# Kernel optimization log

Hardware: AMD Instinct MI355X
Metric: run time of the kernel (lower is better)

## Reference

```python
import jax, jax.numpy as jnp
import numpy as np

B, S, DIM = 4, 1024, 2048
NH, NKV, HD = 16, 4, 128
G = NH // NKV  # query heads per kv head


def _rope(t, cos, sin):
    # t: (B, S, H, HD); cos/sin: (S, HD//2). Llama-style pairwise rotation.
    tr = t.reshape(*t.shape[:-1], HD // 2, 2)
    t_r, t_i = tr[..., 0], tr[..., 1]
    c = cos[None, :, None, :]
    s = sin[None, :, None, :]
    out_r = t_r * c - t_i * s
    out_i = t_r * s + t_i * c
    return jnp.stack([out_r, out_i], axis=-1).reshape(t.shape)


def setup_inputs() -> dict:
    key = jax.random.key(0)
    ks = jax.random.split(key, 5)
    x = jax.random.normal(ks[0], (B, S, DIM), dtype=jnp.float32)
    # Standard RoPE frequencies
    inv_freq = 1.0 / (10000.0 ** (jnp.arange(0, HD, 2, dtype=jnp.float32) / HD))
    ang = jnp.outer(jnp.arange(S, dtype=jnp.float32), inv_freq)  # (S, HD//2)
    freqs_cos = jnp.cos(ang)
    freqs_sin = jnp.sin(ang)
    # Additive causal mask (1,1,S,S)
    causal = jnp.tril(jnp.ones((S, S), dtype=bool))
    attention_mask = jnp.where(causal, 0.0, -1e9).astype(jnp.float32)[None, None]
    sc = 0.02
    wq = jax.random.normal(ks[1], (NH * HD, DIM), dtype=jnp.float32) * sc
    wk = jax.random.normal(ks[2], (NKV * HD, DIM), dtype=jnp.float32) * sc
    wv = jax.random.normal(ks[3], (NKV * HD, DIM), dtype=jnp.float32) * sc
    wo = jax.random.normal(ks[4], (DIM, NH * HD), dtype=jnp.float32) * sc
    return {"x": x, "freqs_cos": freqs_cos, "freqs_sin": freqs_sin,
            "attention_mask": attention_mask, "wq": wq, "wk": wk, "wv": wv, "wo": wo}


def reference(x, freqs_cos, freqs_sin, attention_mask, wq, wk, wv, wo):
    b, s, _ = x.shape
    q = (x @ wq.T).reshape(b, s, NH, HD)
    k = (x @ wk.T).reshape(b, s, NKV, HD)
    v = (x @ wv.T).reshape(b, s, NKV, HD)
    q = _rope(q, freqs_cos, freqs_sin)
    k = _rope(k, freqs_cos, freqs_sin)
    # kv cache (pre-repeat, as in the torch module)
    new_kv_cache = (k, v)
    # GQA attention: broadcast KV heads across query-head groups instead of
    # materializing repeat_kv (identical math).
    qh = q.transpose(0, 2, 1, 3).reshape(b, NKV, G, s, HD)  # (b, kv, g, s, d)
    kh = k.transpose(0, 2, 1, 3)                             # (b, kv, s, d)
    vh = v.transpose(0, 2, 1, 3)
    scale = 1.0 / jnp.sqrt(jnp.asarray(HD, dtype=x.dtype))
    scores = jnp.einsum('bkgqd,bksd->bkgqs', qh, kh) * scale
    scores = scores + attention_mask[:, :, None]  # (1,1,1,S,S) broadcast
    attn = jax.nn.softmax(scores, axis=-1)
    out = jnp.einsum('bkgqs,bksd->bkgqd', attn, vh)
    out = out.reshape(b, NH, s, HD).transpose(0, 2, 1, 3).reshape(b, s, NH * HD)
    out = out @ wo.T
    return (out, new_kv_cache)
```

## Files before the change

### kernel.cpp

```cpp
#include <hip/hip_runtime.h>

typedef __bf16 bf16;
typedef __bf16 bf16x8 __attribute__((ext_vector_type(8)));
typedef __bf16 bf16x4 __attribute__((ext_vector_type(4)));
typedef float  f32x4  __attribute__((ext_vector_type(4)));

#define AS1 __attribute__((address_space(1)))
#define AS3 __attribute__((address_space(3)))

__device__ __forceinline__ void gload16(void* g, void* l) {
  __builtin_amdgcn_global_load_lds((AS1 void*)g, (AS3 void*)l, 16, 0, 0);
}

__global__ void cast_all(const float4* __restrict__ x,  const float4* __restrict__ wq,
                         const float4* __restrict__ wk, const float4* __restrict__ wv,
                         const float4* __restrict__ wo,
                         bf16x4* __restrict__ xb, bf16x4* __restrict__ wqb,
                         bf16x4* __restrict__ wkvb, bf16x4* __restrict__ wob) {
  long i = (long)blockIdx.x * 256 + threadIdx.x;
  float4 v; bf16x4* dp;
  if (i < 2097152)      { v = x[i];            dp = xb + i; }
  else if (i < 3145728) { v = wq[i - 2097152]; dp = wqb + (i - 2097152); }
  else if (i < 3407872) { v = wk[i - 3145728]; dp = wkvb + (i - 3145728); }
  else if (i < 3670016) { v = wv[i - 3407872]; dp = wkvb + 262144 + (i - 3407872); }
  else                  { v = wo[i - 3670016]; dp = wob + (i - 3670016); }
  bf16x4 o;
  o[0] = (bf16)v.x; o[1] = (bf16)v.y; o[2] = (bf16)v.z; o[3] = (bf16)v.w;
  *dp = o;
}

#define PH_OPEN12 \
  asm volatile("s_waitcnt lgkmcnt(8)" ::: "memory"); \
  __builtin_amdgcn_s_barrier(); \
  asm volatile("s_waitcnt lgkmcnt(0)" ::: "memory"); \
  __builtin_amdgcn_sched_barrier(0); \
  __builtin_amdgcn_s_setprio(1);

#define PH_OPEN \
  __builtin_amdgcn_s_barrier(); \
  asm volatile("s_waitcnt lgkmcnt(0)" ::: "memory"); \
  __builtin_amdgcn_sched_barrier(0); \
  __builtin_amdgcn_s_setprio(1);

#define PH_CLOSE \
  __builtin_amdgcn_s_setprio(0); \
  __builtin_amdgcn_sched_barrier(0); \
  __builtin_amdgcn_s_barrier();

#define WVMT() { \
  if constexpr (NFR == 4) { asm volatile("s_waitcnt vmcnt(4)" ::: "memory"); } \
  else if constexpr (NFR == 3) { \
    if (w < 4) { asm volatile("s_waitcnt vmcnt(4)" ::: "memory"); } \
    else       { asm volatile("s_waitcnt vmcnt(2)" ::: "memory"); } \
  } else { asm volatile("s_waitcnt vmcnt(2)" ::: "memory"); } }

#define MFMAQ(q) \
  _Pragma("unroll") for (int kk = 0; kk < 2; kk++) \
  _Pragma("unroll") for (int m2 = 0; m2 < 2; m2++) \
  _Pragma("unroll") for (int ni = 0; ni < NFR; ni++) \
    acc[(q)*2+m2][ni] = __builtin_amdgcn_mfma_f32_16x16x32_bf16(af[m2][kk], bfr[ni][kk], acc[(q)*2+m2][ni], 0, 0, 0);

template<int NFR>
__global__ __launch_bounds__(512, 2) void gemm8(const bf16* __restrict__ A,
                                                const bf16* __restrict__ Bt,
                                                int N, int epi,
                                                float* __restrict__ Cf,
                                                bf16* __restrict__ qbb,
                                                bf16* __restrict__ kbf,
                                                float* __restrict__ kcache,
                                                float* __restrict__ vcache,
                                                bf16* __restrict__ vtb,
                                                const float* __restrict__ fc,
                                                const float* __restrict__ fs) {
  __shared__ __align__(16) char As[2][32768];
  __shared__ __align__(16) char Bs[2][8192 * NFR];
  const int t = threadIdx.x;
  const int w = t >> 6, l = t & 63, lr = l & 15, lh = l >> 4;
  const int wr = w >> 2, wc = w & 3;
  const int m0 = blockIdx.y << 8, n0 = blockIdx.x * (NFR * 64);

  f32x4 acc[8][NFR];
#pragma unroll
  for (int i = 0; i < 8; i++)
#pragma unroll
    for (int j = 0; j < NFR; j++) acc[i][j] = {0.f, 0.f, 0.f, 0.f};

  auto stA = [&](int buf, int half, int kt) {
#pragma unroll
    for (int p = 0; p < 2; p++) {
      int c = t + (p << 9);
      int rl = c >> 3, sl = c & 7, gs = sl ^ (rl & 7);
      gload16((void*)(A + (long)(m0 + (half << 7) + rl) * 2048 + (kt << 6) + (gs << 3)),
              &As[buf][(half << 14) + (c << 4)]);
    }
  };
  auto stB = [&](int buf, int half, int kt) {
    constexpr int CH = NFR * 256;
#pragma unroll
    for (int p = 0; p < (CH + 511) >> 9; p++) {
      int c = t + (p << 9);
      if ((CH & 511) && c >= CH) continue;
      int rl = c >> 3, sl = c & 7, gs = sl ^ (rl & 7);
      gload16((void*)(Bt + (long)(n0 + half * (NFR * 32) + rl) * 2048 + (kt << 6) + (gs << 3)),
              &Bs[buf][half * (NFR * 4096) + (c << 4)]);
    }
  };
  auto rdA = [&](int buf, int mi, int kk) -> bf16x8 {
    int row = (wr << 7) + (mi << 4) + lr;
    int sl  = ((kk << 2) | lh) ^ (row & 7);
    return *(const bf16x8*)(&As[buf][row * 128 + (sl << 4)]);
  };
  auto rdB = [&](int buf, int ni, int kk) -> bf16x8 {
    int row = wc * (NFR * 16) + (ni << 4) + lr;
    int sl  = ((kk << 2) | lh) ^ (row & 7);
    return *(const bf16x8*)(&Bs[buf][row * 128 + (sl << 4)]);
  };

  stB(0, 0, 0); stB(0, 1, 0);
  stA(0, 0, 0); stA(0, 1, 0);
  stB(1, 0, 1); stB(1, 1, 1);
  WVMT();
  __builtin_amdgcn_s_barrier();

  const int NI = 16;
  for (int j = 0; j < NI; j++) {
    const int ktE = 2 * j, ktO = 2 * j + 1;
    const bool last = (j == NI - 1);
    bf16x8 bfr[NFR][2], af[2][2];

#pragma unroll
    for (int ni = 0; ni < NFR; ni++) { bfr[ni][0] = rdB(0, ni, 0); bfr[ni][1] = rdB(0, ni, 1); }
    af[0][0] = rdA(0, 0, 0); af[0][1] = rdA(0, 0, 1);
    af[1][0] = rdA(0, 1, 0); af[1][1] = rdA(0, 1, 1);
    stA(1, 0, ktO);
    PH_OPEN12; MFMAQ(0); PH_CLOSE;

    af[0][0] = rdA(0, 2, 0); af[0][1] = rdA(0, 2, 1);
    af[1][0] = rdA(0, 3, 0); af[1][1] = rdA(0, 3, 1);
    stA(1, 1, ktO);
    PH_OPEN; MFMAQ(1); PH_CLOSE;

    af[0][0] = rdA(0, 4, 0); af[0][1] = rdA(0, 4, 1);
    af[1][0] = rdA(0, 5, 0); af[1][1] = rdA(0, 5, 1);
    if (!last) stB(0, 0, ktE + 2);
    PH_OPEN; MFMAQ(2); PH_CLOSE;

    af[0][0] = rdA(0, 6, 0); af[0][1] = rdA(0, 6, 1);
    af[1][0] = rdA(0, 7, 0); af[1][1] = rdA(0, 7, 1);
    if (!last) stB(0, 1, ktE + 2);
    PH_OPEN; MFMAQ(3);
    __builtin_amdgcn_s_setprio(0);
    __builtin_amdgcn_sched_barrier(0);
    if (last) { asm volatile("s_waitcnt vmcnt(0)" ::: "memory"); }
    else      { WVMT(); }
    __builtin_amdgcn_s_barrier();

#pragma unroll
    for (int ni = 0; ni < NFR; ni++) { bfr[ni][0] = rdB(1, ni, 0); bfr[ni][1] = rdB(1, ni, 1); }
    af[0][0] = rdA(1, 0, 0); af[0][1] = rdA(1, 0, 1);
    af[1][0] = rdA(1, 1, 0); af[1][1] = rdA(1, 1, 1);
    if (!last) stA(0, 0, ktE + 2);
    PH_OPEN12; MFMAQ(0); PH_CLOSE;

    af[0][0] = rdA(1, 2, 0); af[0][1] = rdA(1, 2, 1);
    af[1][0] = rdA(1, 3, 0); af[1][1] = rdA(1, 3, 1);
    if (!last) stA(0, 1, ktE + 2);
    PH_OPEN; MFMAQ(1); PH_CLOSE;

    af[0][0] = rdA(1, 4, 0); af[0][1] = rdA(1, 4, 1);
    af[1][0] = rdA(1, 5, 0); af[1][1] = rdA(1, 5, 1);
    if (!last) stB(1, 0, ktO + 2);
    PH_OPEN; MFMAQ(2); PH_CLOSE;

    af[0][0] = rdA(1, 6, 0); af[0][1] = rdA(1, 6, 1);
    af[1][0] = rdA(1, 7, 0); af[1][1] = rdA(1, 7, 1);
    if (!last) stB(1, 1, ktO + 2);
    PH_OPEN; MFMAQ(3);
    __builtin_amdgcn_s_setprio(0);
    __builtin_amdgcn_sched_barrier(0);
    if (!last) { WVMT(); }
    __builtin_amdgcn_s_barrier();
  }

  const float qs = 0.08838834764831845f;
  const int im = lr & 1;
#pragma unroll
  for (int mi = 0; mi < 8; mi++)
#pragma unroll
    for (int ni = 0; ni < NFR; ni++) {
      int col  = n0 + wc * (NFR * 16) + (ni << 4) + lr;
      int rowb = m0 + (wr << 7) + (mi << 4) + (lh << 2);
      if (epi == 0) {
#pragma unroll
        for (int r = 0; r < 4; r++)
          Cf[(long)(rowb + r) * N + col] = acc[mi][ni][r];
      } else if (col < 2048) {
        int i2 = (col & 127) >> 1;
#pragma unroll
        for (int r = 0; r < 4; r++) {
          int row = rowb + r, s = row & 1023;
          float c = fc[(s << 6) + i2], sn = fs[(s << 6) + i2];
          float own = acc[mi][ni][r], oth = __shfl_xor(own, 1);
          float xr = im ? oth : own, xi = im ? own : oth;
          float val = im ? (xr * sn + xi * c) : (xr * c - xi * sn);
          qbb[(long)row * 2048 + col] = (bf16)(val * qs);
        }
      } else if (col < 2560) {
        int ck = col - 2048;
        int i2 = (ck & 127) >> 1;
#pragma unroll
        for (int r = 0; r < 4; r++) {
          int row = rowb + r, s = row & 1023;
          float c = fc[(s << 6) + i2], sn = fs[(s << 6) + i2];
          float own = acc[mi][ni][r], oth = __shfl_xor(own, 1);
          float xr = im ? oth : own, xi = im ? own : oth;
          float val = im ? (xr * sn + xi * c) : (xr * c - xi * sn);
          kbf[(long)row * 512 + ck] = (bf16)val;
          kcache[(long)row * 512 + ck] = val;
        }
      } else {
        int cv = col - 2560;
        bf16x4 pk;
#pragma unroll
        for (int r = 0; r < 4; r++) {
          float v = acc[mi][ni][r];
          vcache[(long)(rowb + r) * 512 + cv] = v;
          pk[r] = (bf16)v;
        }
        int b = rowb >> 10, s0 = rowb & 1023;
        *(bf16x4*)(vtb + ((long)((b << 2) + (cv >> 7)) * 128 + (cv & 127)) * 1024 + s0) = pk;
      }
    }
}

__global__ __launch_bounds__(256) void attn_k(const bf16* __restrict__ qb,
                                              const bf16* __restrict__ kb,
                                              const bf16* __restrict__ vt,
                                              bf16* __restrict__ aob) {
  const int bh = blockIdx.x;
  const int qt = 15 - blockIdx.y;
  const int b = bh >> 4, h = bh & 15, kv = h >> 2;
  const int t = threadIdx.x, w = t >> 6, l = t & 63, lr = l & 15, lh = l >> 4;
  __shared__ __align__(16) char Ks[2][16384];
  __shared__ __align__(16) char Vs[2][16384];
  __shared__ __align__(16) bf16 Ps[4][16][72];

  bf16x8 qfrag[4];
  {
    const int qrow = (qt << 6) + (w << 4) + lr;
    const bf16* qp = qb + ((long)(b * 1024 + qrow) << 11) + (h << 7);
#pragma unroll
    for (int kc = 0; kc < 4; kc++) qfrag[kc] = *(const bf16x8*)(qp + (kc << 5) + (lh << 3));
  }

  f32x4 acc[8];
#pragma unroll
  for (int i = 0; i < 8; i++) acc[i] = {0.f, 0.f, 0.f, 0.f};
  float m[4]  = {-1e30f, -1e30f, -1e30f, -1e30f};
  float ls[4] = {0.f, 0.f, 0.f, 0.f};

  const bf16* kg = kb + ((long)b << 19) + (kv << 7);
  const bf16* vg = vt + ((long)(b * 4 + kv) << 17);
  const int nt = qt + 1;

  auto stage = [&](int buf, int tt2) {
    const int kv0 = tt2 << 6;
#pragma unroll
    for (int pass = 0; pass < 4; pass++) {
      int c = t + (pass << 8);
      { int row = c >> 4, slot = c & 15, gs = slot ^ (row & 7);
        gload16((void*)(kg + (long)(kv0 + row) * 512 + (gs << 3)), &Ks[buf][c * 16]); }
      { int row = c >> 3, slot = c & 7,  gs = slot ^ (row & 7);
        gload16((void*)(vg + (long)row * 1024 + kv0 + (gs << 3)), &Vs[buf][c * 16]); }
    }
  };

  stage(0, 0);
  int cur = 0;

  for (int tt = 0; tt < nt; tt++) {
    __syncthreads();
    if (tt + 1 < nt) stage(cur ^ 1, tt + 1);

    f32x4 s4[4];
#pragma unroll
    for (int nf = 0; nf < 4; nf++) s4[nf] = {0.f, 0.f, 0.f, 0.f};
    __builtin_amdgcn_s_setprio(1);
#pragma unroll
    for (int nf = 0; nf < 4; nf++) {
      int key = (nf << 4) + lr;
#pragma unroll
      for (int kc = 0; kc < 4; kc++) {
        bf16x8 kf8 = *(const bf16x8*)(&Ks[cur][0] + key * 256 + (((kc << 6) + (lh << 4)) ^ ((key & 7) << 4)));
        s4[nf] = __builtin_amdgcn_mfma_f32_16x16x32_bf16(qfrag[kc], kf8, s4[nf], 0, 0, 0);
      }
    }
    __builtin_amdgcn_s_setprio(0);

    if (tt == qt) {
      const int kv0 = tt << 6;
#pragma unroll
      for (int nf = 0; nf < 4; nf++) {
        int key = kv0 + (nf << 4) + lr;
#pragma unroll
        for (int r = 0; r < 4; r++) {
          int qg = (qt << 6) + (w << 4) + (lh << 2) + r;
          if (key > qg) s4[nf][r] = -1e30f;
        }
      }
    }

    float mc[4];
#pragma unroll
    for (int r = 0; r < 4; r++)
      mc[r] = fmaxf(fmaxf(s4[0][r], s4[1][r]), fmaxf(s4[2][r], s4[3][r]));
#pragma unroll
    for (int d = 1; d < 16; d <<= 1)
#pragma unroll
      for (int r = 0; r < 4; r++) mc[r] = fmaxf(mc[r], __shfl_xor(mc[r], d));

    int grow = 0;
#pragma unroll
    for (int r = 0; r < 4; r++) grow |= (mc[r] > m[r] + 8.f) ? 1 : 0;
    if (__any(grow)) {
      f32x4 av;
#pragma unroll
      for (int r = 0; r < 4; r++) {
        float mn = fmaxf(m[r], mc[r]);
        float al = __expf(m[r] - mn);
        m[r] = mn; ls[r] *= al; av[r] = al;
      }
#pragma unroll
      for (int hf = 0; hf < 8; hf++) acc[hf] *= av;
    }

    float rs[4] = {0.f, 0.f, 0.f, 0.f};
#pragma unroll
    for (int nf = 0; nf < 4; nf++)
#pragma unroll
      for (int r = 0; r < 4; r++) {
        float p = __expf(s4[nf][r] - m[r]);
        s4[nf][r] = p;
        rs[r] += p;
      }
#pragma unroll
    for (int d = 1; d < 16; d <<= 1)
#pragma unroll
      for (int r = 0; r < 4; r++) rs[r] += __shfl_xor(rs[r], d);
#pragma unroll
    for (int r = 0; r < 4; r++) ls[r] += rs[r];

#pragma unroll
    for (int nf = 0; nf < 4; nf++)
#pragma unroll
      for (int r = 0; r < 4; r++)
        Ps[w][(lh << 2) + r][(nf << 4) + lr] = (bf16)s4[nf][r];

    __builtin_amdgcn_s_setprio(1);
#pragma unroll
    for (int kc = 0; kc < 2; kc++) {
      bf16x8 pf8 = *(const bf16x8*)((const char*)&Ps[w][lr][0] + (kc << 6) + (lh << 4));
#pragma unroll
      for (int hf = 0; hf < 8; hf++) {
        int hd = (hf << 4) + lr;
        bf16x8 vf8 = *(const bf16x8*)(&Vs[cur][0] + hd * 128 + (((kc << 6) + (lh << 4)) ^ ((hd & 7) << 4)));
        acc[hf] = __builtin_amdgcn_mfma_f32_16x16x32_bf16(pf8, vf8, acc[hf], 0, 0, 0);
      }
    }
    __builtin_amdgcn_s_setprio(0);
    cur ^= 1;
  }

  float inv[4];
#pragma unroll
  for (int r = 0; r < 4; r++) inv[r] = 1.f / ls[r];
#pragma unroll
  for (int hf = 0; hf < 8; hf++)
#pragma unroll
    for (int r = 0; r < 4; r++) {
      int qrow = (qt << 6) + (w << 4) + (lh << 2) + r;
      aob[((long)(b * 1024 + qrow) << 11) + (h << 7) + (hf << 4) + lr] = (bf16)(acc[hf][r] * inv[r]);
    }
}

extern "C" void kernel_launch(void* const* d_in, const int* in_sizes, int n_in,
                              void* d_out, int out_size, void* d_ws, size_t ws_size,
                              hipStream_t stream) {
  (void)in_sizes; (void)n_in; (void)out_size; (void)ws_size;
  const float* x  = (const float*)d_in[0];
  const float* fc = (const float*)d_in[1];
  const float* fs = (const float*)d_in[2];
  const float* wq = (const float*)d_in[4];
  const float* wk = (const float*)d_in[5];
  const float* wv = (const float*)d_in[6];
  const float* wo = (const float*)d_in[7];

  float* out    = (float*)d_out;
  float* kcache = out + 8388608;
  float* vcache = out + 10485760;

  char* ws = (char*)d_ws;
  bf16* xb    = (bf16*)(ws);
  bf16* wqkv  = (bf16*)(ws + 16777216);
  bf16* wob   = (bf16*)(ws + 29360128);
  bf16* qbb   = (bf16*)(ws + 54525952);
  bf16* kbf   = (bf16*)(ws + 71303168);
  bf16* vtb   = (bf16*)(ws + 75497472);
  bf16* aob   = (bf16*)(ws + 79691776);

  cast_all<<<18432, 256, 0, stream>>>((const float4*)x, (const float4*)wq,
                                      (const float4*)wk, (const float4*)wv,
                                      (const float4*)wo,
                                      (bf16x4*)xb, (bf16x4*)wqkv,
                                      (bf16x4*)(wqkv + 4194304), (bf16x4*)wob);

  gemm8<3><<<dim3(16, 16), 512, 0, stream>>>(xb, wqkv, 3072, 1, nullptr,
                                             qbb, kbf, kcache, vcache, vtb, fc, fs);

  attn_k<<<dim3(64, 16), 256, 0, stream>>>(qbb, kbf, vtb, aob);

  gemm8<2><<<dim3(16, 16), 512, 0, stream>>>(aob, wob, 2048, 0, out,
                                             nullptr, nullptr, nullptr, nullptr, nullptr,
                                             nullptr, nullptr);
}
```

Before: 171.7 us.

## Double-buffer GEMM fragment registers to overlap LDS reads with MFMA

Restructures the main GEMM loop so A and B fragments are ping-ponged between two register sets, so LDS reads for the next quarter run while MFMAs consume the current one. Prefetch of the first fragments is moved before the loop, global load issue points and vmcnt waits are rebalanced, and the per-phase barrier is moved to the close of each phase. This aims to hide LDS latency behind matrix math, at the cost of more VGPRs under a 512-thread, 2-wave occupancy bound and a tighter sync ordering that could race if the waits are miscounted.

```diff
diff --git a/kernel.cpp b/kernel.cpp
--- a/kernel.cpp
+++ b/kernel.cpp
@@ -29,36 +29,45 @@
   *dp = o;
 }
 
-#define PH_OPEN12 \
-  asm volatile("s_waitcnt lgkmcnt(8)" ::: "memory"); \
-  __builtin_amdgcn_s_barrier(); \
+#define OPEN() \
   asm volatile("s_waitcnt lgkmcnt(0)" ::: "memory"); \
+  __builtin_amdgcn_sched_barrier(0);
+
+#define MID() \
   __builtin_amdgcn_sched_barrier(0); \
   __builtin_amdgcn_s_setprio(1);
 
-#define PH_OPEN \
-  __builtin_amdgcn_s_barrier(); \
-  asm volatile("s_waitcnt lgkmcnt(0)" ::: "memory"); \
-  __builtin_amdgcn_sched_barrier(0); \
-  __builtin_amdgcn_s_setprio(1);
-
-#define PH_CLOSE \
+#define CLOSE() \
   __builtin_amdgcn_s_setprio(0); \
   __builtin_amdgcn_sched_barrier(0); \
   __builtin_amdgcn_s_barrier();
 
-#define WVMT() { \
-  if constexpr (NFR == 4) { asm volatile("s_waitcnt vmcnt(4)" ::: "memory"); } \
-  else if constexpr (NFR == 3) { \
-    if (w < 4) { asm volatile("s_waitcnt vmcnt(4)" ::: "memory"); } \
-    else       { asm volatile("s_waitcnt vmcnt(2)" ::: "memory"); } \
-  } else { asm volatile("s_waitcnt vmcnt(2)" ::: "memory"); } }
-
-#define MFMAQ(q) \
+#define WVMP() { \
+  if (last) { asm volatile("s_waitcnt vmcnt(0)" ::: "memory"); } \
+  else { \
+    if constexpr (NFR == 3) { \
+      if (w < 4) { asm volatile("s_waitcnt vmcnt(2)" ::: "memory"); } \
+      else       { asm volatile("s_waitcnt vmcnt(1)" ::: "memory"); } \
+    } else if constexpr (NFR == 4) { \
+      asm volatile("s_waitcnt vmcnt(2)" ::: "memory"); \
+    } else { \
+      asm volatile("s_waitcnt vmcnt(1)" ::: "memory"); \
+    } \
+  } }
+
+#define MFMAQ(q, AF, BF) \
   _Pragma("unroll") for (int kk = 0; kk < 2; kk++) \
   _Pragma("unroll") for (int m2 = 0; m2 < 2; m2++) \
   _Pragma("unroll") for (int ni = 0; ni < NFR; ni++) \
-    acc[(q)*2+m2][ni] = __builtin_amdgcn_mfma_f32_16x16x32_bf16(af[m2][kk], bfr[ni][kk], acc[(q)*2+m2][ni], 0, 0, 0);
+    acc[(q)*2+m2][ni] = __builtin_amdgcn_mfma_f32_16x16x32_bf16(AF[m2][kk], BF[ni][kk], acc[(q)*2+m2][ni], 0, 0, 0);
+
+#define RD_A2(AF, buf, q) \
+  AF[0][0] = rdA(buf, 2*(q),   0); AF[0][1] = rdA(buf, 2*(q),   1); \
+  AF[1][0] = rdA(buf, 2*(q)+1, 0); AF[1][1] = rdA(buf, 2*(q)+1, 1);
+
+#define RD_B(BF, buf) \
+  _Pragma("unroll") for (int ni = 0; ni < NFR; ni++) { \
+    BF[ni][0] = rdB(buf, ni, 0); BF[ni][1] = rdB(buf, ni, 1); }
 
 template<int NFR>
 __global__ __launch_bounds__(512, 2) void gemm8(const bf16* __restrict__ A,
@@ -116,70 +125,79 @@
     return *(const bf16x8*)(&Bs[buf][row * 128 + (sl << 4)]);
   };
 
+  bf16x8 afX[2][2], afY[2][2], bfrX[NFR][2], bfrY[NFR][2];
+
   stB(0, 0, 0); stB(0, 1, 0);
   stA(0, 0, 0); stA(0, 1, 0);
   stB(1, 0, 1); stB(1, 1, 1);
-  WVMT();
+  if constexpr (NFR == 3) {
+    if (w < 4) { asm volatile("s_waitcnt vmcnt(4)" ::: "memory"); }
+    else       { asm volatile("s_waitcnt vmcnt(2)" ::: "memory"); }
+  } else if constexpr (NFR == 4) {
+    asm volatile("s_waitcnt vmcnt(4)" ::: "memory");
+  } else {
+    asm volatile("s_waitcnt vmcnt(2)" ::: "memory");
+  }
   __builtin_amdgcn_s_barrier();
+  RD_B(bfrX, 0);
+  RD_A2(afX, 0, 0);
 
   const int NI = 16;
   for (int j = 0; j < NI; j++) {
-    const int ktE = 2 * j, ktO = 2 * j + 1;
     const bool last = (j == NI - 1);
-    bf16x8 bfr[NFR][2], af[2][2];
-
-#pragma unroll
-    for (int ni = 0; ni < NFR; ni++) { bfr[ni][0] = rdB(0, ni, 0); bfr[ni][1] = rdB(0, ni, 1); }
-    af[0][0] = rdA(0, 0, 0); af[0][1] = rdA(0, 0, 1);
-    af[1][0] = rdA(0, 1, 0); af[1][1] = rdA(0, 1, 1);
+    const int ktO = 2 * j + 1;
+
+    OPEN();
+    RD_A2(afY, 0, 1);
     stA(1, 0, ktO);
-    PH_OPEN12; MFMAQ(0); PH_CLOSE;
-
-    af[0][0] = rdA(0, 2, 0); af[0][1] = rdA(0, 2, 1);
-    af[1][0] = rdA(0, 3, 0); af[1][1] = rdA(0, 3, 1);
+    MID(); MFMAQ(0, afX, bfrX); CLOSE();
+
+    OPEN();
+    RD_A2(afX, 0, 2);
     stA(1, 1, ktO);
-    PH_OPEN; MFMAQ(1); PH_CLOSE;
-
-    af[0][0] = rdA(0, 4, 0); af[0][1] = rdA(0, 4, 1);
-    af[1][0] = rdA(0, 5, 0); af[1][1] = rdA(0, 5, 1);
-    if (!last) stB(0, 0, ktE + 2);
-    PH_OPEN; MFMAQ(2); PH_CLOSE;
-
-    af[0][0] = rdA(0, 6, 0); af[0][1] = rdA(0, 6, 1);
-    af[1][0] = rdA(0, 7, 0); af[1][1] = rdA(0, 7, 1);
-    if (!last) stB(0, 1, ktE + 2);
-    PH_OPEN; MFMAQ(3);
+    MID(); MFMAQ(1, afY, bfrX); CLOSE();
+
+    OPEN();
+    RD_A2(afY, 0, 3);
+    if (!last) stB(0, 0, ktO + 1);
+    MID(); MFMAQ(2, afX, bfrX);
     __builtin_amdgcn_s_setprio(0);
     __builtin_amdgcn_sched_barrier(0);
-    if (last) { asm volatile("s_waitcnt vmcnt(0)" ::: "memory"); }
-    else      { WVMT(); }
+    WVMP();
     __builtin_amdgcn_s_barrier();
 
-#pragma unroll
-    for (int ni = 0; ni < NFR; ni++) { bfr[ni][0] = rdB(1, ni, 0); bfr[ni][1] = rdB(1, ni, 1); }
-    af[0][0] = rdA(1, 0, 0); af[0][1] = rdA(1, 0, 1);
-    af[1][0] = rdA(1, 1, 0); af[1][1] = rdA(1, 1, 1);
-    if (!last) stA(0, 0, ktE + 2);
-    PH_OPEN12; MFMAQ(0); PH_CLOSE;
-
-    af[0][0] = rdA(1, 2, 0); af[0][1] = rdA(1, 2, 1);
-    af[1][0] = rdA(1, 3, 0); af[1][1] = rdA(1, 3, 1);
-    if (!last) stA(0, 1, ktE + 2);
-    PH_OPEN; MFMAQ(1); PH_CLOSE;
-
-    af[0][0] = rdA(1, 4, 0); af[0][1] = rdA(1, 4, 1);
-    af[1][0] = rdA(1, 5, 0); af[1][1] = rdA(1, 5, 1);
+    OPEN();
+    RD_B(bfrY, 1);
+    RD_A2(afX, 1, 0);
+    if (!last) stB(0, 1, ktO + 1);
+    MID(); MFMAQ(3, afY, bfrX); CLOSE();
+
+    OPEN();
+    RD_A2(afY, 1, 1);
+    if (!last) stA(0, 0, ktO + 1);
+    MID(); MFMAQ(0, afX, bfrY); CLOSE();
+
+    OPEN();
+    RD_A2(afX, 1, 2);
+    if (!last) stA(0, 1, ktO + 1);
+    MID(); MFMAQ(1, afY, bfrY); CLOSE();
+
+    OPEN();
+    RD_A2(afY, 1, 3);
     if (!last) stB(1, 0, ktO + 2);
-    PH_OPEN; MFMAQ(2); PH_CLOSE;
-
-    af[0][0] = rdA(1, 6, 0); af[0][1] = rdA(1, 6, 1);
-    af[1][0] = rdA(1, 7, 0); af[1][1] = rdA(1, 7, 1);
-    if (!last) stB(1, 1, ktO + 2);
-    PH_OPEN; MFMAQ(3);
+    MID(); MFMAQ(2, afX, bfrY);
     __builtin_amdgcn_s_setprio(0);
     __builtin_amdgcn_sched_barrier(0);
-    if (!last) { WVMT(); }
+    WVMP();
     __builtin_amdgcn_s_barrier();
+
+    OPEN();
+    if (!last) {
+      RD_B(bfrX, 0);
+      RD_A2(afX, 0, 0);
+      stB(1, 1, ktO + 2);
+    }
+    MID(); MFMAQ(3, afY, bfrY); CLOSE();
   }
 
   const float qs = 0.08838834764831845f;
```

New measurement: 174.4 us. Within noise of the previous version (+1.5%).
